# Optimization experiments

Hardware: AMD Instinct MI355X
Metric: run time of the kernel (lower is better)

The kernel has to match this reference:

```python
import jax, jax.numpy as jnp
import numpy as np

BN_EPS = 1e-5


def _bn(x, g, b, m, v):
    # inference-mode BatchNorm2d over channel axis 1 of [B,C,F,T]
    scale = (g * jax.lax.rsqrt(v + BN_EPS))[None, :, None, None]
    shift = (b - g * m * jax.lax.rsqrt(v + BN_EPS))[None, :, None, None]
    return x * scale + shift


def _prelu(x, a):
    return jnp.where(x > 0, x, a[None, :, None, None] * x)


def _conv1x1(x, w):
    # w: [out, in]; x: [B,C,F,T]
    return jnp.einsum('oc,bcft->boft', w, x)


def setup_inputs() -> dict:
    key = jax.random.key(0)
    ks = jax.random.split(key, 8)
    B, C, F, T = 4, 64, 256, 400
    d_c = C // 4  # 16
    inp = jax.random.normal(ks[0], (B, C, F, T), dtype=jnp.float32)
    # causal time mask: True = masked (future frames)
    mask = jnp.triu(jnp.ones((T, T), dtype=bool), k=1)[None, None]  # [1,1,T,T]
    w_fqkv = jax.random.normal(ks[1], (3 * d_c, C), dtype=jnp.float32) / np.sqrt(C)
    w_tqk = jax.random.normal(ks[2], (2 * d_c, C), dtype=jnp.float32) / np.sqrt(C)
    w_proj = jax.random.normal(ks[3], (C, d_c), dtype=jnp.float32) / np.sqrt(d_c)
    def bn_params(k, n):
        k1, k2 = jax.random.split(k)
        return (1.0 + 0.1 * jax.random.normal(k1, (n,), dtype=jnp.float32),
                0.1 * jax.random.normal(k2, (n,), dtype=jnp.float32),
                0.1 * jax.random.normal(jax.random.fold_in(k, 7), (n,), dtype=jnp.float32),
                jnp.abs(1.0 + 0.1 * jax.random.normal(jax.random.fold_in(k, 9), (n,), dtype=jnp.float32)))
    g1, b1, m1, v1 = bn_params(ks[4], 3 * d_c)
    g2, b2, m2, v2 = bn_params(ks[5], 2 * d_c)
    g3, b3, m3, v3 = bn_params(ks[6], C)
    a1 = 0.25 * jnp.ones((3 * d_c,), dtype=jnp.float32)
    a2 = 0.25 * jnp.ones((2 * d_c,), dtype=jnp.float32)
    a3 = 0.25 * jnp.ones((C,), dtype=jnp.float32)
    return dict(inp=inp, mask=mask, w_fqkv=w_fqkv, g1=g1, b1=b1, m1=m1, v1=v1, a1=a1,
                w_tqk=w_tqk, g2=g2, b2=b2, m2=m2, v2=v2, a2=a2,
                w_proj=w_proj, g3=g3, b3=b3, m3=m3, v3=v3, a3=a3)


def reference(inp, mask, w_fqkv, g1, b1, m1, v1, a1,
              w_tqk, g2, b2, m2, v2, a2,
              w_proj, g3, b3, m3, v3, a3):
    d_c = w_proj.shape[1]
    scale = 1.0 / np.sqrt(d_c).astype(np.float32)
    # frequency attention
    f_qkv = _prelu(_bn(_conv1x1(inp, w_fqkv), g1, b1, m1, v1), a1)  # [B,3d,F,T]
    qf, kf, v = f_qkv[:, :d_c], f_qkv[:, d_c:2 * d_c], f_qkv[:, 2 * d_c:]
    f_score = jnp.einsum('bcft,bcyt->btfy', qf, kf) * scale
    f_score = jax.nn.softmax(f_score, axis=-1)
    f_out = jnp.einsum('btfy,bcyt->bcft', f_score, v)
    # time attention
    t_qk = _prelu(_bn(_conv1x1(inp, w_tqk), g2, b2, m2, v2), a2)  # [B,2d,F,T]
    qt, kt = t_qk[:, :d_c], t_qk[:, d_c:]
    t_score = jnp.einsum('bcft,bcfy->bfty', qt, kt) * scale
    neg = -jnp.finfo(t_score.dtype).max
    t_score = jnp.where(mask, neg, t_score)
    t_score = jax.nn.softmax(t_score, axis=-1)
    t_out = jnp.einsum('bfty,bcfy->bcft', t_score, f_out)
    out = _prelu(_bn(_conv1x1(t_out, w_proj), g3, b3, m3, v3), a3)
    return out + inp
```

## Files before the change

### kernel.cpp

```cpp
#include <hip/hip_runtime.h>
#include <hip/hip_bf16.h>

#define B_ 4
#define C_ 64
#define F_ 256
#define T_ 400
#define DC 16
#define NB 102400

typedef __hip_bfloat16 bf16;
typedef __attribute__((ext_vector_type(8))) short bf16x8s;
typedef __attribute__((ext_vector_type(4))) short short4v;
typedef __attribute__((ext_vector_type(4))) float f32x4;
typedef __attribute__((ext_vector_type(2))) short short2v;

__device__ __forceinline__ float b2f(bf16 x){ return __bfloat162float(x); }
__device__ __forceinline__ bf16  f2b(float x){ return __float2bfloat16(x); }
__device__ __forceinline__ short f2bs(float x){ bf16 h = __float2bfloat16(x); short s; __builtin_memcpy(&s,&h,2); return s; }

#define MFMA16(a,b,c) __builtin_amdgcn_mfma_f32_16x16x32_bf16((a),(b),(c),0,0,0)

__global__ __launch_bounds__(256) void k_proj(
    const float* __restrict__ inp,
    const float* __restrict__ w_fqkv,
    const float* __restrict__ g1, const float* __restrict__ b1,
    const float* __restrict__ m1, const float* __restrict__ v1,
    const float* __restrict__ a1,
    const float* __restrict__ w_tqk,
    const float* __restrict__ g2, const float* __restrict__ b2,
    const float* __restrict__ m2, const float* __restrict__ v2,
    const float* __restrict__ a2,
    bf16* __restrict__ qf, bf16* __restrict__ kf, bf16* __restrict__ vv,
    bf16* __restrict__ qt, bf16* __restrict__ kt)
{
    __shared__ short Xs[256*72];
    __shared__ short Ws[80*72];
    __shared__ float sc[80], sh[80], al[80];

    const int tid = threadIdx.x;
    const int b   = blockIdx.x / 400;
    const int n0  = (blockIdx.x - b*400) * 256;

    for (int i = tid; i < 80*32; i += 256) {
        int o = i >> 5, cp = (i & 31) * 2;
        const float* src = (o < 48) ? &w_fqkv[o*64 + cp] : &w_tqk[(o-48)*64 + cp];
        short2v wv; wv.x = f2bs(src[0]); wv.y = f2bs(src[1]);
        *(short2v*)&Ws[o*72 + cp] = wv;
    }
    if (tid < 48) {
        float rs = rsqrtf(v1[tid] + 1e-5f);
        float g  = g1[tid];
        sc[tid] = g * rs;
        sh[tid] = b1[tid] - g * m1[tid] * rs;
        al[tid] = a1[tid];
    }
    if (tid >= 128 && tid < 160) {
        int o = tid - 128;
        float rs = rsqrtf(v2[o] + 1e-5f);
        float g  = g2[o];
        sc[48+o] = g * rs;
        sh[48+o] = b2[o] - g * m2[o] * rs;
        al[48+o] = a2[o];
    }
    {
        const float* xb = inp + (size_t)b*64*NB + n0 + tid;
        #pragma unroll 4
        for (int cp = 0; cp < 32; cp++) {
            float x0 = xb[(size_t)(2*cp  )*NB];
            float x1 = xb[(size_t)(2*cp+1)*NB];
            short2v xv; xv.x = f2bs(x0); xv.y = f2bs(x1);
            *(short2v*)&Xs[tid*72 + 2*cp] = xv;
        }
    }
    __syncthreads();

    const int wave = tid >> 6;
    const int lane = tid & 63;
    const int ln   = lane & 15;
    const int quad = lane >> 4;
    const f32x4 zero = {0.f,0.f,0.f,0.f};

    bf16x8s Bf[4][2];
    #pragma unroll
    for (int nt = 0; nt < 4; nt++) {
        int nl = wave*64 + nt*16 + ln;
        Bf[nt][0] = *(const bf16x8s*)&Xs[nl*72 + quad*8];
        Bf[nt][1] = *(const bf16x8s*)&Xs[nl*72 + 32 + quad*8];
    }

    #pragma unroll
    for (int mt = 0; mt < 5; mt++) {
        bf16x8s A0 = *(const bf16x8s*)&Ws[(mt*16+ln)*72 + quad*8];
        bf16x8s A1 = *(const bf16x8s*)&Ws[(mt*16+ln)*72 + 32 + quad*8];
        float scv[4], shv[4], alv[4];
        #pragma unroll
        for (int r = 0; r < 4; r++) {
            int o = mt*16 + quad*4 + r;
            scv[r] = sc[o]; shv[r] = sh[o]; alv[r] = al[o];
        }
        #pragma unroll
        for (int nt = 0; nt < 4; nt++) {
            f32x4 acc = MFMA16(A0, Bf[nt][0], zero);
            acc = MFMA16(A1, Bf[nt][1], acc);
            short4v hs;
            #pragma unroll
            for (int r = 0; r < 4; r++) {
                float y = acc[r]*scv[r] + shv[r];
                y = y > 0.f ? y : alv[r]*y;
                if (mt == 0 || mt == 3) y *= 0.25f;
                hs[r] = f2bs(y);
            }
            const int n = n0 + wave*64 + nt*16 + ln;
            const int f = n / T_;
            const int t = n - f*T_;
            if (mt < 3) {
                size_t idx = (((size_t)b*T_ + t)*F_ + f)*DC + quad*4;
                bf16* dst = (mt == 0) ? qf : (mt == 1) ? kf : vv;
                *(short4v*)((short*)dst + idx) = hs;
            } else {
                size_t idx = (((size_t)b*F_ + f)*T_ + t)*DC + quad*4;
                bf16* dst = (mt == 3) ? qt : kt;
                *(short4v*)((short*)dst + idx) = hs;
            }
        }
    }
}

__global__ __launch_bounds__(256) void k_fattn(
    const bf16* __restrict__ qf, const bf16* __restrict__ kf,
    const bf16* __restrict__ vv, bf16* __restrict__ fout)
{
    __shared__ short Ks[F_*24];
    __shared__ short Vt[16*264];
    __shared__ short Pb[4][16*72];

    const int bt = blockIdx.x;
    const int b = bt / T_, t = bt - b*T_;
    const size_t base = ((size_t)b*T_ + t)*F_*DC;
    const short* kfp = (const short*)(kf + base);
    const short* vvp = (const short*)(vv + base);
    const short* qfp = (const short*)(qf + base);
    const int tid = threadIdx.x;

    for (int i = tid; i < F_*8; i += 256) {
        int r = i >> 3, cp = (i & 7) * 2;
        short2v v = *(const short2v*)&kfp[r*16+cp];
        *(short2v*)&Ks[r*24+cp] = v;
    }
    for (int i = tid; i < F_*8; i += 256) {
        int f = i >> 3, cp = (i & 7) * 2;
        short2v v = *(const short2v*)&vvp[f*16+cp];
        Vt[cp*264 + f]     = v.x;
        Vt[(cp+1)*264 + f] = v.y;
    }
    __syncthreads();

    const int wave = tid >> 6;
    const int lane = tid & 63;
    const int ln   = lane & 15;
    const int quad = lane >> 4;
    short* Pw = &Pb[wave][0];
    const f32x4 zero = {0.f,0.f,0.f,0.f};

    for (int s = wave; s < F_/16; s += 4) {
        bf16x8s A = {};
        if (quad < 2) A = *(const bf16x8s*)&qfp[(s*16+ln)*16 + quad*8];

        f32x4 sum = zero, O = zero;
        for (int ch = 0; ch < 4; ch++) {
            #pragma unroll
            for (int i2 = 0; i2 < 4; i2++) {
                int yt = ch*4 + i2;
                bf16x8s Bf = {};
                if (quad < 2) Bf = *(const bf16x8s*)&Ks[(yt*16+ln)*24 + quad*8];
                f32x4 S = MFMA16(A, Bf, zero);
                #pragma unroll
                for (int r = 0; r < 4; r++) {
                    float p = __expf(S[r]);
                    sum[r] += p;
                    Pw[(quad*4+r)*72 + i2*16 + ln] = f2bs(p);
                }
            }
            #pragma unroll
            for (int h = 0; h < 2; h++) {
                bf16x8s Pa = *(const bf16x8s*)&Pw[ln*72 + h*32 + quad*8];
                bf16x8s Vb = *(const bf16x8s*)&Vt[ln*264 + ch*64 + h*32 + quad*8];
                O = MFMA16(Pa, Vb, O);
            }
        }
        #pragma unroll
        for (int m = 1; m < 16; m <<= 1) {
            #pragma unroll
            for (int r = 0; r < 4; r++) sum[r] += __shfl_xor(sum[r], m, 64);
        }
        #pragma unroll
        for (int r = 0; r < 4; r++) {
            int f = s*16 + quad*4 + r;
            fout[(((size_t)b*F_ + f)*T_ + t)*DC + ln] = f2b(O[r]/sum[r]);
        }
    }
}

__global__ __launch_bounds__(256) void k_tattn(
    const bf16* __restrict__ qt, const bf16* __restrict__ kt,
    const bf16* __restrict__ fo, bf16* __restrict__ tout)
{
    __shared__ short Ks[T_*24];
    __shared__ short Vt[16*456];
    __shared__ short Pb[4][16*72];

    const int bfi = blockIdx.x;
    const int b = bfi / F_, f = bfi - b*F_;
    const size_t base = ((size_t)b*F_ + f)*T_*DC;
    const short* ktp = (const short*)(kt + base);
    const short* fop = (const short*)(fo + base);
    const short* qtp = (const short*)(qt + base);
    const int tid = threadIdx.x;

    for (int i = tid; i < T_*8; i += 256) {
        int r = i >> 3, cp = (i & 7) * 2;
        short2v v = *(const short2v*)&ktp[r*16+cp];
        *(short2v*)&Ks[r*24+cp] = v;
    }
    for (int i = tid; i < T_*8; i += 256) {
        int y = i >> 3, cp = (i & 7) * 2;
        short2v v = *(const short2v*)&fop[y*16+cp];
        Vt[cp*456 + y]     = v.x;
        Vt[(cp+1)*456 + y] = v.y;
    }
    for (int i = tid; i < 16*64; i += 256) {
        int c = i >> 6, y = T_ + (i & 63);
        if (y < 456) Vt[c*456 + y] = 0;
    }
    __syncthreads();

    const int wave = tid >> 6;
    const int lane = tid & 63;
    const int ln   = lane & 15;
    const int quad = lane >> 4;
    short* Pw = &Pb[wave][0];
    const f32x4 zero = {0.f,0.f,0.f,0.f};

    for (int s = wave; s < 25; s += 4) {
        bf16x8s A = {};
        if (quad < 2) A = *(const bf16x8s*)&qtp[(s*16+ln)*16 + quad*8];

        f32x4 sum = zero, O = zero;
        const int nch = (s + 4) >> 2;
        for (int ch = 0; ch < nch; ch++) {
            #pragma unroll
            for (int i2 = 0; i2 < 4; i2++) {
                int yt = ch*4 + i2;
                if (yt <= s) {
                    bf16x8s Bf = {};
                    if (quad < 2) Bf = *(const bf16x8s*)&Ks[(yt*16+ln)*24 + quad*8];
                    f32x4 S = MFMA16(A, Bf, zero);
                    const bool diag = (yt == s);
                    #pragma unroll
                    for (int r = 0; r < 4; r++) {
                        float p = __expf(S[r]);
                        if (diag && ln > quad*4+r) p = 0.f;
                        sum[r] += p;
                        Pw[(quad*4+r)*72 + i2*16 + ln] = f2bs(p);
                    }
                } else {
                    #pragma unroll
                    for (int r = 0; r < 4; r++)
                        Pw[(quad*4+r)*72 + i2*16 + ln] = 0;
                }
            }
            #pragma unroll
            for (int h = 0; h < 2; h++) {
                bf16x8s Pa = *(const bf16x8s*)&Pw[ln*72 + h*32 + quad*8];
                bf16x8s Vb = *(const bf16x8s*)&Vt[ln*456 + ch*64 + h*32 + quad*8];
                O = MFMA16(Pa, Vb, O);
            }
        }
        #pragma unroll
        for (int m = 1; m < 16; m <<= 1) {
            #pragma unroll
            for (int r = 0; r < 4; r++) sum[r] += __shfl_xor(sum[r], m, 64);
        }
        #pragma unroll
        for (int r = 0; r < 4; r++) {
            int t = s*16 + quad*4 + r;
            tout[base + (size_t)t*DC + ln] = f2b(O[r]/sum[r]);
        }
    }
}

__global__ __launch_bounds__(256) void k_proj2(
    const bf16* __restrict__ tog, const float* __restrict__ w_proj,
    const float* __restrict__ g3, const float* __restrict__ b3,
    const float* __restrict__ m3, const float* __restrict__ v3,
    const float* __restrict__ a3,
    const float* __restrict__ inp, float* __restrict__ out)
{
    __shared__ short Ws2[64*24];
    __shared__ float sc[64], sh[64], al[64];

    const int tid = threadIdx.x;
    const int b   = blockIdx.x / 400;
    const int n0  = (blockIdx.x - b*400) * 256;

    for (int i = tid; i < 64*8; i += 256) {
        int o = i >> 3, cp = (i & 7) * 2;
        short2v wv; wv.x = f2bs(w_proj[o*16+cp]); wv.y = f2bs(w_proj[o*16+cp+1]);
        *(short2v*)&Ws2[o*24 + cp] = wv;
    }
    if (tid < 64) {
        float rs = rsqrtf(v3[tid] + 1e-5f);
        float g  = g3[tid];
        sc[tid] = g * rs;
        sh[tid] = b3[tid] - g * m3[tid] * rs;
        al[tid] = a3[tid];
    }
    __syncthreads();

    const int wave = tid >> 6;
    const int lane = tid & 63;
    const int ln   = lane & 15;
    const int quad = lane >> 4;
    const f32x4 zero = {0.f,0.f,0.f,0.f};
    const short* top = (const short*)tog + (size_t)b*NB*DC;

    bf16x8s Bf[4];
    #pragma unroll
    for (int nt = 0; nt < 4; nt++) {
        Bf[nt] = (bf16x8s){};
        if (quad < 2) {
            int n = n0 + wave*64 + nt*16 + ln;
            Bf[nt] = *(const bf16x8s*)&top[(size_t)n*DC + quad*8];
        }
    }

    #pragma unroll
    for (int mt = 0; mt < 4; mt++) {
        bf16x8s A = {};
        if (quad < 2) A = *(const bf16x8s*)&Ws2[(mt*16+ln)*24 + quad*8];
        float scv[4], shv[4], alv[4];
        #pragma unroll
        for (int r = 0; r < 4; r++) {
            int o = mt*16 + quad*4 + r;
            scv[r] = sc[o]; shv[r] = sh[o]; alv[r] = al[o];
        }
        #pragma unroll
        for (int nt = 0; nt < 4; nt++) {
            f32x4 acc = MFMA16(A, Bf[nt], zero);
            const int n = n0 + wave*64 + nt*16 + ln;
            #pragma unroll
            for (int r = 0; r < 4; r++) {
                int o = mt*16 + quad*4 + r;
                float y = acc[r]*scv[r] + shv[r];
                y = y > 0.f ? y : alv[r]*y;
                size_t gi = ((size_t)b*64 + o)*NB + n;
                out[gi] = y + inp[gi];
            }
        }
    }
}

extern "C" void kernel_launch(void* const* d_in, const int* in_sizes, int n_in,
                              void* d_out, int out_size, void* d_ws, size_t ws_size,
                              hipStream_t stream)
{
    const float* inp    = (const float*)d_in[0];
    const float* w_fqkv = (const float*)d_in[2];
    const float* g1 = (const float*)d_in[3],  *b1 = (const float*)d_in[4];
    const float* m1 = (const float*)d_in[5],  *v1 = (const float*)d_in[6];
    const float* a1 = (const float*)d_in[7];
    const float* w_tqk  = (const float*)d_in[8];
    const float* g2 = (const float*)d_in[9],  *b2 = (const float*)d_in[10];
    const float* m2 = (const float*)d_in[11], *v2 = (const float*)d_in[12];
    const float* a2 = (const float*)d_in[13];
    const float* w_proj = (const float*)d_in[14];
    const float* g3 = (const float*)d_in[15], *b3 = (const float*)d_in[16];
    const float* m3 = (const float*)d_in[17], *v3 = (const float*)d_in[18];
    const float* a3 = (const float*)d_in[19];
    float* out = (float*)d_out;

    const size_t NQ = (size_t)B_*T_*F_*DC;
    bf16* ws = (bf16*)d_ws;
    bf16 *qf = ws,        *kf = ws + NQ,   *vv = ws + 2*NQ;
    bf16 *qt = ws + 3*NQ, *kt = ws + 4*NQ;
    bf16 *fo = ws + 5*NQ, *to = ws + 6*NQ;

    k_proj <<<B_*400, 256, 0, stream>>>(inp, w_fqkv, g1,b1,m1,v1,a1,
                                        w_tqk, g2,b2,m2,v2,a2,
                                        qf, kf, vv, qt, kt);
    k_fattn<<<B_*T_, 256, 0, stream>>>(qf, kf, vv, fo);
    k_tattn<<<B_*F_, 256, 0, stream>>>(qt, kt, fo, to);
    k_proj2<<<B_*400, 256, 0, stream>>>(to, w_proj, g3,b3,m3,v3,a3, inp, out);
}
```

Measured before the change: 392.6 us.

## Tile projection kernel as 16x16 (f,t) blocks with swizzled shared layout

The projection kernel now processes a 16x16 tile in frequency and time instead of 256 contiguous flattened positions. Input is loaded with float4 vector reads and stored to shared memory under an XOR swizzle. Two B-fragment sets are built, one per output layout, so that both the frequency-major (qf/kf/v) and time-major (qt/kt) stores write contiguous 16-element runs. This targets the scattered global writes and the scalar input loads, at the cost of more register pressure and more complex indexing.

New measurement: 376.5 us. 4.1% less time.

```diff
diff --git a/kernel.cpp b/kernel.cpp
--- a/kernel.cpp
+++ b/kernel.cpp
@@ -33,13 +33,16 @@
     bf16* __restrict__ qf, bf16* __restrict__ kf, bf16* __restrict__ vv,
     bf16* __restrict__ qt, bf16* __restrict__ kt)
 {
-    __shared__ short Xs[256*72];
+    __shared__ short Xs[256*64];
     __shared__ short Ws[80*72];
     __shared__ float sc[80], sh[80], al[80];
 
     const int tid = threadIdx.x;
-    const int b   = blockIdx.x / 400;
-    const int n0  = (blockIdx.x - b*400) * 256;
+    const int blk = blockIdx.x;
+    const int b   = blk / 400;
+    const int rem = blk - b*400;
+    const int f0  = (rem & 15) * 16;
+    const int t0  = (rem >> 4) * 16;
 
     for (int i = tid; i < 80*32; i += 256) {
         int o = i >> 5, cp = (i & 31) * 2;
@@ -62,14 +65,22 @@
         sh[48+o] = b2[o] - g * m2[o] * rs;
         al[48+o] = a2[o];
     }
+
     {
-        const float* xb = inp + (size_t)b*64*NB + n0 + tid;
-        #pragma unroll 4
-        for (int cp = 0; cp < 32; cp++) {
-            float x0 = xb[(size_t)(2*cp  )*NB];
-            float x1 = xb[(size_t)(2*cp+1)*NB];
-            short2v xv; xv.x = f2bs(x0); xv.y = f2bs(x1);
-            *(short2v*)&Xs[tid*72 + 2*cp] = xv;
+        const int wv = tid >> 6, lnn = tid & 63;
+        const int fi = lnn >> 2, tc = lnn & 3;
+        const float* xb = inp + (size_t)b*64*NB + (size_t)(f0+fi)*T_ + t0 + tc*4;
+        #pragma unroll
+        for (int p = 0; p < 16; p++) {
+            const int c = p*4 + wv;
+            f32x4 x = *(const f32x4*)&xb[(size_t)c*NB];
+            const int chi = c >> 3, clo = c & 7;
+            #pragma unroll
+            for (int j = 0; j < 4; j++) {
+                int r = (tc*4 + j)*16 + fi;
+                int slot = chi ^ (r & 7) ^ ((r >> 4) & 7);
+                Xs[r*64 + slot*8 + clo] = f2bs(x[j]);
+            }
         }
     }
     __syncthreads();
@@ -80,12 +91,23 @@
     const int quad = lane >> 4;
     const f32x4 zero = {0.f,0.f,0.f,0.f};
 
-    bf16x8s Bf[4][2];
+    bf16x8s B1[4][2];
+    bf16x8s B2[4][2];
     #pragma unroll
     for (int nt = 0; nt < 4; nt++) {
-        int nl = wave*64 + nt*16 + ln;
-        Bf[nt][0] = *(const bf16x8s*)&Xs[nl*72 + quad*8];
-        Bf[nt][1] = *(const bf16x8s*)&Xs[nl*72 + 32 + quad*8];
+        const int tile = wave*4 + nt;
+        {
+            const int r  = tile*16 + ln;
+            const int sw = (ln & 7) ^ (tile & 7);
+            B1[nt][0] = *(const bf16x8s*)&Xs[r*64 + ((quad     ^ sw) * 8)];
+            B1[nt][1] = *(const bf16x8s*)&Xs[r*64 + (((4+quad) ^ sw) * 8)];
+        }
+        {
+            const int r  = ln*16 + tile;
+            const int sw = (tile & 7) ^ (ln & 7);
+            B2[nt][0] = *(const bf16x8s*)&Xs[r*64 + ((quad     ^ sw) * 8)];
+            B2[nt][1] = *(const bf16x8s*)&Xs[r*64 + (((4+quad) ^ sw) * 8)];
+        }
     }
 
     #pragma unroll
@@ -100,8 +122,10 @@
         }
         #pragma unroll
         for (int nt = 0; nt < 4; nt++) {
-            f32x4 acc = MFMA16(A0, Bf[nt][0], zero);
-            acc = MFMA16(A1, Bf[nt][1], acc);
+            bf16x8s Bb0 = (mt < 3) ? B1[nt][0] : B2[nt][0];
+            bf16x8s Bb1 = (mt < 3) ? B1[nt][1] : B2[nt][1];
+            f32x4 acc = MFMA16(A0, Bb0, zero);
+            acc = MFMA16(A1, Bb1, acc);
             short4v hs;
             #pragma unroll
             for (int r = 0; r < 4; r++) {
@@ -110,15 +134,13 @@
                 if (mt == 0 || mt == 3) y *= 0.25f;
                 hs[r] = f2bs(y);
             }
-            const int n = n0 + wave*64 + nt*16 + ln;
-            const int f = n / T_;
-            const int t = n - f*T_;
+            const int tile = wave*4 + nt;
             if (mt < 3) {
-                size_t idx = (((size_t)b*T_ + t)*F_ + f)*DC + quad*4;
+                size_t idx = (((size_t)b*T_ + (t0+tile))*F_ + (f0+ln))*DC + quad*4;
                 bf16* dst = (mt == 0) ? qf : (mt == 1) ? kf : vv;
                 *(short4v*)((short*)dst + idx) = hs;
             } else {
-                size_t idx = (((size_t)b*F_ + f)*T_ + t)*DC + quad*4;
+                size_t idx = (((size_t)b*F_ + (f0+tile))*T_ + (t0+ln))*DC + quad*4;
                 bf16* dst = (mt == 3) ? qt : kt;
                 *(short4v*)((short*)dst + idx) = hs;
             }
```
